# Kernel optimization log

Hardware: AMD Instinct MI355X
Metric: run time of the kernel (lower is better)

The kernel has to match this reference:

```python
import jax, jax.numpy as jnp
import numpy as np

N, E, F_IN, HID, HEADS, G = 50000, 800000, 128, 128, 4, 512
NEG_SLOPE = 0.2


def setup_inputs() -> dict:
    key = jax.random.key(0)
    ks = jax.random.split(key, 16)
    x = jax.random.normal(ks[0], (N, F_IN), dtype=jnp.float32)
    edge_index = jax.random.randint(ks[1], (2, E), 0, N, dtype=jnp.int32)
    batch = jnp.sort(jax.random.randint(ks[2], (N,), 0, G, dtype=jnp.int32))
    s1 = 1.0 / np.sqrt(F_IN)
    s2 = 1.0 / np.sqrt(HEADS * HID)
    params = {
        "W1": jax.random.uniform(ks[3], (F_IN, HEADS * HID), jnp.float32, -s1, s1),
        "a_src1": jax.random.normal(ks[4], (HEADS, HID), jnp.float32) * s1,
        "a_dst1": jax.random.normal(ks[5], (HEADS, HID), jnp.float32) * s1,
        "b1": jnp.zeros((HEADS * HID,), jnp.float32),
        "W2": jax.random.uniform(ks[6], (HEADS * HID, HID), jnp.float32, -s2, s2),
        "a_src2": jax.random.normal(ks[7], (1, HID), jnp.float32) * s2,
        "a_dst2": jax.random.normal(ks[8], (1, HID), jnp.float32) * s2,
        "b2": jnp.zeros((HID,), jnp.float32),
        "Wl": jax.random.normal(ks[9], (HID, 1), jnp.float32) / np.sqrt(HID),
        "bl": jnp.zeros((1,), jnp.float32),
    }
    return dict(x=x, edge_index=edge_index, batch=batch, **params)


def _gat_conv(x, W, a_src, a_dst, b, src, dst, heads, out_ch):
    n = x.shape[0]
    h = (x @ W).reshape(n, heads, out_ch)                      # [N,H,C]
    asrc = jnp.sum(h * a_src, axis=-1)                          # [N,H]
    adst = jnp.sum(h * a_dst, axis=-1)                          # [N,H]
    logits = jax.nn.leaky_relu(asrc[src] + adst[dst], NEG_SLOPE)  # [E,H]
    m = jax.ops.segment_max(logits, dst, num_segments=n)        # stable softmax per dst
    e = jnp.exp(logits - m[dst])
    denom = jax.ops.segment_sum(e, dst, num_segments=n)
    alpha = e / denom[dst]                                      # [E,H]
    out = jax.ops.segment_sum(alpha[:, :, None] * h[src], dst, num_segments=n)
    return out.reshape(n, heads * out_ch) + b


def reference(x, edge_index, batch, W1, a_src1, a_dst1, b1, W2, a_src2, a_dst2, b2, Wl, bl):
    n = x.shape[0]
    loop = jnp.arange(n, dtype=edge_index.dtype)
    src = jnp.concatenate([edge_index[0], loop])  # add_self_loops=True (PyG default)
    dst = jnp.concatenate([edge_index[1], loop])
    h = _gat_conv(x, W1, a_src1, a_dst1, b1, src, dst, HEADS, HID)
    h = jax.nn.elu(h)
    h = _gat_conv(h, W2, a_src2, a_dst2, b2, src, dst, 1, HID)
    h = jax.nn.elu(h)
    # global_mean_pool
    sums = jax.ops.segment_sum(h, batch, num_segments=G)
    cnts = jax.ops.segment_sum(jnp.ones((n,), h.dtype), batch, num_segments=G)
    pooled = sums / jnp.maximum(cnts, 1.0)[:, None]
    return (pooled @ Wl + bl).squeeze()
```

## Files before the change

### kernel.cpp

```cpp
#include <hip/hip_runtime.h>
#include <math.h>

#define NEG_SLOPE 0.2f

typedef float f4 __attribute__((ext_vector_type(4)));
typedef __attribute__((ext_vector_type(8))) short short8;
typedef __attribute__((ext_vector_type(4))) float f32x4;
typedef unsigned short ushort_t;
typedef unsigned char uchar_t;

__device__ __forceinline__ float bf2f(unsigned short s) {
    unsigned u = ((unsigned)s) << 16;
    float f; __builtin_memcpy(&f, &u, 4); return f;
}
__device__ __forceinline__ unsigned short f2bf(float f) {
    unsigned u; __builtin_memcpy(&u, &f, 4);
    u = (u + 0x7FFFu + ((u >> 16) & 1u)) >> 16;
    return (unsigned short)u;
}
__device__ __forceinline__ void gload16(const void* g, void* l) {
    __builtin_amdgcn_global_load_lds((const __attribute__((address_space(1))) void*)g,
                                     (__attribute__((address_space(3))) void*)l, 16, 0, 0);
}
__device__ __forceinline__ void cvt4(unsigned u, float& a, float& b, float& c, float& d) {
    asm("v_cvt_f32_ubyte0 %0, %1" : "=v"(a) : "v"(u));
    asm("v_cvt_f32_ubyte1 %0, %1" : "=v"(b) : "v"(u));
    asm("v_cvt_f32_ubyte2 %0, %1" : "=v"(c) : "v"(u));
    asm("v_cvt_f32_ubyte3 %0, %1" : "=v"(d) : "v"(u));
}

__global__ void prep_kernel(const float* __restrict__ x, const float* __restrict__ W1,
                            const float* __restrict__ W2, ushort_t* __restrict__ xb,
                            ushort_t* __restrict__ W1t, ushort_t* __restrict__ W2t,
                            const int* __restrict__ ei, int* __restrict__ deg,
                            int n_x, int pad_x, int E, int Et) {
    int i = blockIdx.x * blockDim.x + threadIdx.x;
    if (i < Et) {
        int d = (i < E) ? ei[E + i] : (i - E);
        atomicAdd(&deg[d], 1);
    }
    if (i < pad_x) {
        xb[i] = f2bf(i < n_x ? x[i] : 0.f);
        return;
    }
    int k = i - pad_x;
    if (k < 128 * 512) {
        int r = k >> 9, c = k & 511;
        W1t[(size_t)c * 128 + r] = f2bf(W1[k]);
        return;
    }
    k -= 128 * 512;
    if (k < 512 * 128) {
        int r = k >> 7, c = k & 127;
        W2t[(size_t)c * 512 + r] = f2bf(W2[k]);
    }
}

__global__ __launch_bounds__(1024) void scan_local(const int* __restrict__ deg,
                                                   int* __restrict__ off,
                                                   int* __restrict__ btot, int n) {
    __shared__ int s_w[16];
    int tid = threadIdx.x, lane = tid & 63, wv = tid >> 6;
    int i = blockIdx.x * 1024 + tid;
    int v = (i < n) ? deg[i] : 0;
    int x = v;
    #pragma unroll
    for (int d = 1; d < 64; d <<= 1) {
        int y = __shfl_up(x, d);
        if (lane >= d) x += y;
    }
    if (lane == 63) s_w[wv] = x;
    __syncthreads();
    if (tid < 16) {
        int y = s_w[tid];
        int z = y;
        #pragma unroll
        for (int d = 1; d < 16; d <<= 1) {
            int t2 = __shfl_up(z, d);
            if (tid >= d) z += t2;
        }
        if (tid == 15) btot[blockIdx.x] = z;
        s_w[tid] = z - y;
    }
    __syncthreads();
    if (i < n) off[i] = s_w[wv] + (x - v);
}

__global__ __launch_bounds__(256) void scan_add(const int* __restrict__ btot,
                                                int* __restrict__ off,
                                                int* __restrict__ cur,
                                                const int* __restrict__ batch,
                                                int* __restrict__ gcnt, int n, int nb) {
    __shared__ int s_b[2];
    int i = blockIdx.x * 256 + threadIdx.x;
    if (threadIdx.x < 64) {
        int lane = threadIdx.x;
        int v = (lane < nb) ? btot[lane] : 0;
        int x = v;
        #pragma unroll
        for (int d = 1; d < 64; d <<= 1) {
            int y = __shfl_up(x, d);
            if (lane >= d) x += y;
        }
        int c = blockIdx.x >> 2;
        int base = (c == 0) ? 0 : __shfl(x, c - 1);
        int total = __shfl(x, nb - 1);
        if (lane == 0) { s_b[0] = base; s_b[1] = total; }
    }
    __syncthreads();
    if (i < n) {
        int o = off[i] + s_b[0];
        off[i] = o;
        cur[i] = o;
        atomicAdd(&gcnt[batch[i]], 1);
    } else if (i == n) {
        off[n] = s_b[1];
    }
}

__global__ void scatter_kernel(const int* __restrict__ ei, int E, int Et,
                               int* __restrict__ cur, int* __restrict__ csr) {
    int e = blockIdx.x * blockDim.x + threadIdx.x;
    if (e >= Et) return;
    int s, d;
    if (e < E) { s = ei[e]; d = ei[E + e]; }
    else       { s = d = e - E; }
    int p = atomicAdd(&cur[d], 1);
    csr[p] = s;
}

template<int MI, int H>
__global__ __launch_bounds__(256) void gemm_q(const ushort_t* __restrict__ A,
                                              const ushort_t* __restrict__ Bt,
                                              uchar_t* __restrict__ Cq,
                                              const float* __restrict__ aw_src,
                                              const float* __restrict__ aw_dst,
                                              float* __restrict__ side,
                                              float* __restrict__ avd,
                                              int K) {
    constexpr int BM = MI * 32;
    constexpr int AI = MI / 2;
    const int Nc = H * 128;
    __shared__ __align__(16) ushort_t As[BM * 32];
    __shared__ __align__(16) ushort_t Bs[128 * 32];
    __shared__ float s_red[3][2][BM];
    __shared__ float s_rs[BM];
    __shared__ __align__(16) uchar_t s_q[BM * 144];
    const int t = threadIdx.x, w = t >> 6, lane = t & 63;
    const int r0 = blockIdx.x * BM, hb = blockIdx.y, c0 = hb * 128;
    const int wr = w & 1, wc = w >> 1;

    const ushort_t* Ag = A + (size_t)(r0 + w * (BM / 4) + (lane >> 2)) * K + (lane & 3) * 8;
    const ushort_t* Bg = Bt + (size_t)(c0 + w * 32 + (lane >> 2)) * K + (lane & 3) * 8;
    ushort_t* Al = As + w * (BM / 4) * 32;
    ushort_t* Bl = Bs + w * 1024;

    f32x4 acc[MI][4] = {};
    for (int k0 = 0; k0 < K; k0 += 32) {
        __syncthreads();
        #pragma unroll
        for (int m = 0; m < AI; m++) gload16(Ag + k0 + (size_t)m * 16 * K, Al + m * 512);
        gload16(Bg + k0, Bl);
        gload16(Bg + k0 + (size_t)16 * K, Bl + 512);
        __syncthreads();
        short8 af[MI], bf[4];
        #pragma unroll
        for (int i = 0; i < MI; i++)
            af[i] = *(const short8*)(As + (wr * MI * 16 + i * 16 + (lane & 15)) * 32 + (lane >> 4) * 8);
        #pragma unroll
        for (int jj = 0; jj < 4; jj++)
            bf[jj] = *(const short8*)(Bs + (wc * 64 + jj * 16 + (lane & 15)) * 32 + (lane >> 4) * 8);
        #pragma unroll
        for (int i = 0; i < MI; i++)
            #pragma unroll
            for (int jj = 0; jj < 4; jj++)
                acc[i][jj] = __builtin_amdgcn_mfma_f32_16x16x32_bf16(af[i], bf[jj], acc[i][jj], 0, 0, 0);
    }

    float asc[4], adc[4];
    #pragma unroll
    for (int jj = 0; jj < 4; jj++) {
        int c = c0 + wc * 64 + jj * 16 + (lane & 15);
        asc[jj] = aw_src[c];
        adc[jj] = aw_dst[c];
    }
    #pragma unroll
    for (int i = 0; i < MI; i++) {
        #pragma unroll
        for (int r = 0; r < 4; r++) {
            float m = 0.f, ps = 0.f, pd = 0.f;
            #pragma unroll
            for (int jj = 0; jj < 4; jj++) {
                float v = acc[i][jj][r];
                m = fmaxf(m, fabsf(v));
                ps = fmaf(v, asc[jj], ps);
                pd = fmaf(v, adc[jj], pd);
            }
            #pragma unroll
            for (int d = 1; d < 16; d <<= 1) {
                m = fmaxf(m, __shfl_xor(m, d));
                ps += __shfl_xor(ps, d);
                pd += __shfl_xor(pd, d);
            }
            if ((lane & 15) == 0) {
                int row = wr * MI * 16 + i * 16 + (lane >> 4) * 4 + r;
                s_red[0][wc][row] = m;
                s_red[1][wc][row] = ps;
                s_red[2][wc][row] = pd;
            }
        }
    }
    __syncthreads();
    if (t < BM) {
        float rm = fmaxf(fmaxf(s_red[0][0][t], s_red[0][1][t]), 1e-30f);
        s_rs[t] = 127.f / rm;
        int node = r0 + t;
        side[(size_t)node * (2 * H) + hb]     = s_red[1][0][t] + s_red[1][1][t];
        side[(size_t)node * (2 * H) + H + hb] = rm * (1.f / 127.f);
        avd[(size_t)node * H + hb]            = s_red[2][0][t] + s_red[2][1][t];
    }
    __syncthreads();
    #pragma unroll
    for (int i = 0; i < MI; i++)
        #pragma unroll
        for (int jj = 0; jj < 4; jj++)
            #pragma unroll
            for (int r = 0; r < 4; r++) {
                int row = wr * MI * 16 + i * 16 + (lane >> 4) * 4 + r;
                int col = wc * 64 + jj * 16 + (lane & 15);
                int qi = (int)rintf(acc[i][jj][r] * s_rs[row]) + 128;
                qi = min(255, max(0, qi));
                s_q[row * 144 + col] = (uchar_t)qi;
            }
    __syncthreads();
    #pragma unroll
    for (int p2 = 0; p2 < BM / 32; p2++) {
        int idx = p2 * 256 + t;
        int row = idx >> 3, ch = idx & 7;
        *(uint4*)(Cq + (size_t)(r0 + row) * Nc + c0 + ch * 16) =
            *(const uint4*)(s_q + row * 144 + ch * 16);
    }
}

template<int H, int TOT>
__global__ __launch_bounds__(256) void agg_q(const int* __restrict__ off,
                                             const int* __restrict__ csr,
                                             const uchar_t* __restrict__ fq,
                                             const float* __restrict__ side,
                                             const float* __restrict__ avd,
                                             const float* __restrict__ bias,
                                             ushort_t* __restrict__ outb,
                                             float* __restrict__ outf, int n) {
    constexpr int J = TOT / 64;
    __shared__ __align__(16) float2 s_w[4][64 * H];
    int w = threadIdx.x >> 6, lane = threadIdx.x & 63;
    int dst = blockIdx.x * 4 + w;
    if (dst >= n) return;
    float adv[H];
    if constexpr (H == 4) {
        f4 t4 = *(const f4*)&avd[(size_t)dst * 4];
        #pragma unroll
        for (int h = 0; h < 4; h++) adv[h] = t4[h];
    } else {
        adv[0] = avd[dst];
    }
    int beg = off[dst], end = off[dst + 1];
    float den = 0.f, Ssum = 0.f;
    float acc[16] = {};
    float2* eww = s_w[w];

    const int half = lane >> 5, sub32 = lane & 31;
    const int hch  = sub32 >> 3;
    const int slot = lane >> 3, sub8 = lane & 7;

    for (int b = beg; b < end; b += 64) {
        int idx = b + lane;
        bool val = idx < end;
        int sv = val ? csr[idx] : 0;
        unsigned myoff = (unsigned)sv * TOT;
        int cnt = min(64, end - b);

        if constexpr (J == 8) {
            uint4 A[4], B[4];
            auto issue = [&](int p0, uint4* buf) {
                #pragma unroll
                for (int q = 0; q < 4; q++) {
                    unsigned o = (unsigned)__shfl((int)myoff, (p0 + q) * 2 + half);
                    buf[q] = *(const uint4*)(fq + o + sub32 * 16);
                }
            };
            int np = (cnt + 1) >> 1;
            int ng = (np + 3) >> 2;
            issue(0, A);
            {
                const f4* sp = (const f4*)(side + (size_t)sv * 8);
                f4 av = sp[0], sc = sp[1];
                f4 ev, esv;
                #pragma unroll
                for (int h = 0; h < 4; h++) {
                    float l = av[h] + adv[h];
                    l = fmaxf(l, l * NEG_SLOPE);
                    float e = val ? __expf(l) : 0.f;
                    ev[h] = e;
                    esv[h] = e * sc[h];
                }
                f4 v01 = {ev[0], esv[0], ev[1], esv[1]};
                f4 v23 = {ev[2], esv[2], ev[3], esv[3]};
                *(f4*)&eww[lane * 4]     = v01;
                *(f4*)&eww[lane * 4 + 2] = v23;
            }
            asm volatile("s_waitcnt lgkmcnt(0)" ::: "memory");
            auto proc = [&](int p0, uint4* buf) {
                #pragma unroll
                for (int q = 0; q < 4; q++) {
                    float2 ees = eww[((p0 + q) * 2 + half) * 4 + hch];
                    den += ees.x; Ssum += ees.y;
                    float es = ees.y;
                    float b0, b1, b2, b3;
                    cvt4(buf[q].x, b0, b1, b2, b3);
                    acc[0] = fmaf(es, b0, acc[0]);  acc[1] = fmaf(es, b1, acc[1]);
                    acc[2] = fmaf(es, b2, acc[2]);  acc[3] = fmaf(es, b3, acc[3]);
                    cvt4(buf[q].y, b0, b1, b2, b3);
                    acc[4] = fmaf(es, b0, acc[4]);  acc[5] = fmaf(es, b1, acc[5]);
                    acc[6] = fmaf(es, b2, acc[6]);  acc[7] = fmaf(es, b3, acc[7]);
                    cvt4(buf[q].z, b0, b1, b2, b3);
                    acc[8] = fmaf(es, b0, acc[8]);  acc[9] = fmaf(es, b1, acc[9]);
                    acc[10] = fmaf(es, b2, acc[10]); acc[11] = fmaf(es, b3, acc[11]);
                    cvt4(buf[q].w, b0, b1, b2, b3);
                    acc[12] = fmaf(es, b0, acc[12]); acc[13] = fmaf(es, b1, acc[13]);
                    acc[14] = fmaf(es, b2, acc[14]); acc[15] = fmaf(es, b3, acc[15]);
                }
            };
            int g = 0;
            for (;;) {
                if (g + 1 < ng) issue((g + 1) * 4, B);
                proc(g * 4, A);
                if (++g >= ng) break;
                if (g + 1 < ng) issue((g + 1) * 4, A);
                proc(g * 4, B);
                if (++g >= ng) break;
            }
        } else {
            {
                float2 sp = *(const float2*)(side + (size_t)sv * 2);
                float l = sp.x + adv[0];
                l = fmaxf(l, l * NEG_SLOPE);
                float e = val ? __expf(l) : 0.f;
                eww[lane] = make_float2(e, e * sp.y);
            }
            asm volatile("s_waitcnt lgkmcnt(0)" ::: "memory");
            int ng = (cnt + 7) >> 3;
            uint4 bufs[8];
            #pragma unroll
            for (int g = 0; g < 8; g++) {
                if (g < ng) {
                    unsigned o = (unsigned)__shfl((int)myoff, g * 8 + slot);
                    bufs[g] = *(const uint4*)(fq + o + sub8 * 16);
                }
            }
            #pragma unroll
            for (int g = 0; g < 8; g++) {
                if (g < ng) {
                    float2 ees = eww[g * 8 + slot];
                    den += ees.x; Ssum += ees.y;
                    float es = ees.y;
                    float b0, b1, b2, b3;
                    cvt4(bufs[g].x, b0, b1, b2, b3);
                    acc[0] = fmaf(es, b0, acc[0]);  acc[1] = fmaf(es, b1, acc[1]);
                    acc[2] = fmaf(es, b2, acc[2]);  acc[3] = fmaf(es, b3, acc[3]);
                    cvt4(bufs[g].y, b0, b1, b2, b3);
                    acc[4] = fmaf(es, b0, acc[4]);  acc[5] = fmaf(es, b1, acc[5]);
                    acc[6] = fmaf(es, b2, acc[6]);  acc[7] = fmaf(es, b3, acc[7]);
                    cvt4(bufs[g].z, b0, b1, b2, b3);
                    acc[8] = fmaf(es, b0, acc[8]);  acc[9] = fmaf(es, b1, acc[9]);
                    acc[10] = fmaf(es, b2, acc[10]); acc[11] = fmaf(es, b3, acc[11]);
                    cvt4(bufs[g].w, b0, b1, b2, b3);
                    acc[12] = fmaf(es, b0, acc[12]); acc[13] = fmaf(es, b1, acc[13]);
                    acc[14] = fmaf(es, b2, acc[14]); acc[15] = fmaf(es, b3, acc[15]);
                }
            }
        }
    }

    if constexpr (J == 8) {
        den += __shfl_xor(den, 32);
        Ssum += __shfl_xor(Ssum, 32);
        #pragma unroll
        for (int u = 0; u < 16; u++) acc[u] += __shfl_xor(acc[u], 32);
        float rden = 1.f / den;
        if (half == 0) {
            unsigned short ov[16];
            #pragma unroll
            for (int u = 0; u < 16; u++) {
                float v = (acc[u] - 128.f * Ssum) * rden + bias[sub32 * 16 + u];
                v = v > 0.f ? v : expm1f(v);
                ov[u] = f2bf(v);
            }
            ushort_t* op = outb + (size_t)dst * TOT + sub32 * 16;
            *(short8*)op = *(short8*)ov;
            *(short8*)(op + 8) = *(short8*)(ov + 8);
        }
    } else {
        #pragma unroll
        for (int d = 8; d < 64; d <<= 1) {
            den += __shfl_xor(den, d);
            Ssum += __shfl_xor(Ssum, d);
        }
        #pragma unroll
        for (int u = 0; u < 16; u++) {
            #pragma unroll
            for (int d = 8; d < 64; d <<= 1) acc[u] += __shfl_xor(acc[u], d);
        }
        float rden = 1.f / den;
        if (lane < 8) {
            float ov[16];
            #pragma unroll
            for (int u = 0; u < 16; u++) {
                float v = (acc[u] - 128.f * Ssum) * rden + bias[lane * 16 + u];
                ov[u] = v > 0.f ? v : expm1f(v);
            }
            float* op = outf + (size_t)dst * TOT + lane * 16;
            #pragma unroll
            for (int q = 0; q < 4; q++)
                *(f4*)(op + q * 4) = *(f4*)(ov + q * 4);
        }
    }
}

__global__ __launch_bounds__(256) void pool_kernel(const float* __restrict__ feat,
                                                   const int* __restrict__ batch,
                                                   float* __restrict__ gsum, int n) {
    int t = threadIdx.x;
    int ch = t & 127, half = t >> 7;
    int base = blockIdx.x * 64;
    float acc = 0.f;
    int curg = -1;
    for (int k = half; k < 64; k += 2) {
        int node = base + k;
        if (node >= n) break;
        int g = batch[node];
        if (g != curg) {
            if (curg >= 0) atomicAdd(&gsum[(size_t)curg * 128 + ch], acc);
            acc = 0.f;
            curg = g;
        }
        acc += feat[(size_t)node * 128 + ch];
    }
    if (curg >= 0) atomicAdd(&gsum[(size_t)curg * 128 + ch], acc);
}

__global__ __launch_bounds__(256) void final_kernel(const float* __restrict__ gsum,
                                                    const int* __restrict__ gcnt,
                                                    const float* __restrict__ Wl,
                                                    const float* __restrict__ bl,
                                                    float* __restrict__ out, int g_total) {
    int w = threadIdx.x >> 6, lane = threadIdx.x & 63;
    int g = blockIdx.x * 4 + w;
    if (g >= g_total) return;
    float inv = 1.f / fmaxf((float)gcnt[g], 1.f);
    float p = 0.f;
    #pragma unroll
    for (int j = 0; j < 2; j++) {
        int ch = lane + 64 * j;
        p += gsum[(size_t)g * 128 + ch] * Wl[ch];
    }
    #pragma unroll
    for (int d = 32; d; d >>= 1) p += __shfl_xor(p, d);
    if (lane == 0) out[g] = p * inv + bl[0];
}

extern "C" void kernel_launch(void* const* d_in, const int* in_sizes, int n_in,
                              void* d_out, int out_size, void* d_ws, size_t ws_size,
                              hipStream_t stream) {
    const float* x   = (const float*)d_in[0];
    const int*   ei  = (const int*)d_in[1];
    const int*   bat = (const int*)d_in[2];
    const float* W1  = (const float*)d_in[3];
    const float* as1 = (const float*)d_in[4];
    const float* ad1 = (const float*)d_in[5];
    const float* b1  = (const float*)d_in[6];
    const float* W2  = (const float*)d_in[7];
    const float* as2 = (const float*)d_in[8];
    const float* ad2 = (const float*)d_in[9];
    const float* b2  = (const float*)d_in[10];
    const float* Wl  = (const float*)d_in[11];
    const float* bl  = (const float*)d_in[12];
    float* out = (float*)d_out;

    const int N    = in_sizes[0] / 128;
    const int E    = in_sizes[1] / 2;
    const int Et   = E + N;
    const int G    = 512;
    const int Mpad = (N + 127) & ~127;
    const int nb   = (N + 1023) >> 10;

    char* p = (char*)d_ws;
    auto alloc = [&](size_t bytes) { char* r = p; p += (bytes + 255) & ~(size_t)255; return r; };
    ushort_t* xb    = (ushort_t*)alloc((size_t)Mpad * 128 * 2);
    ushort_t* W1t   = (ushort_t*)alloc((size_t)512 * 128 * 2);
    ushort_t* W2t   = (ushort_t*)alloc((size_t)128 * 512 * 2);
    uchar_t*  h1q   = (uchar_t*)alloc((size_t)Mpad * 512);
    ushort_t* hb    = (ushort_t*)alloc((size_t)Mpad * 512 * 2);
    uchar_t*  h2q   = (uchar_t*)alloc((size_t)Mpad * 128);
    float*    feat2 = (float*)alloc((size_t)N * 128 * 4);
    float*    side1 = (float*)alloc((size_t)Mpad * 8 * 4);
    float*    avd1  = (float*)alloc((size_t)Mpad * 4 * 4);
    float*    side2 = (float*)alloc((size_t)Mpad * 2 * 4);
    float*    avd2  = (float*)alloc((size_t)Mpad * 4);
    float*    gsum  = (float*)alloc((size_t)G * 128 * 4);
    int*      gcnt  = (int*)alloc((size_t)G * 4);
    int*      deg   = (int*)alloc((size_t)N * 4);
    int*      off   = (int*)alloc((size_t)(N + 1) * 4);
    int*      cur   = (int*)alloc((size_t)N * 4);
    int*      btot  = (int*)alloc((size_t)128 * 4);
    int*      csr   = (int*)alloc((size_t)Et * 4);

    hipMemsetAsync(gsum, 0, (size_t)((char*)off - (char*)gsum), stream);
    hipMemsetAsync(hb + (size_t)N * 512, 0, (size_t)(Mpad - N) * 512 * 2, stream);

    const int prep_n = Mpad * 128 + 2 * 65536;
    prep_kernel<<<(prep_n + 255) / 256, 256, 0, stream>>>(x, W1, W2, xb, W1t, W2t,
                                                          ei, deg, N * 128, Mpad * 128, E, Et);
    scan_local<<<nb, 1024, 0, stream>>>(deg, off, btot, N);
    scan_add<<<(N + 256) / 256, 256, 0, stream>>>(btot, off, cur, bat, gcnt, N, nb);
    scatter_kernel<<<(Et + 255) / 256, 256, 0, stream>>>(ei, E, Et, cur, csr);

    gemm_q<4, 4><<<dim3(Mpad / 128, 4), 256, 0, stream>>>(xb, W1t, h1q, as1, ad1, side1, avd1, 128);
    agg_q<4, 512><<<(N + 3) / 4, 256, 0, stream>>>(off, csr, h1q, side1, avd1, b1, hb, nullptr, N);

    gemm_q<2, 1><<<dim3(Mpad / 64, 1), 256, 0, stream>>>(hb, W2t, h2q, as2, ad2, side2, avd2, 512);
    agg_q<1, 128><<<(N + 3) / 4, 256, 0, stream>>>(off, csr, h2q, side2, avd2, b2, nullptr, feat2, N);

    pool_kernel<<<(N + 63) / 64, 256, 0, stream>>>(feat2, bat, gsum, N);
    final_kernel<<<(G + 3) / 4, 256, 0, stream>>>(gsum, gcnt, Wl, bl, out, G);
}
```

Baseline: 513.3 us.

## Store layer-1 quantized features head-major and split aggregation per head

The layer-1 GEMM now writes int8 features in a head-major layout ([H][Mpad][128]) and interleaves side data per head. Layer-1 aggregation is split across a grid y-dimension of 4 heads, each warp gathering 128-byte rows for one head instead of 512-byte rows for all heads. This shrinks the gathered working set per launch so it fits cache better and adds parallelism. In exchange, the CSR indices and side data are reread four times and the double-buffered prefetch pipeline is replaced by simpler batched loads.

```diff
diff --git a/kernel.cpp b/kernel.cpp
--- a/kernel.cpp
+++ b/kernel.cpp
@@ -9,10 +9,6 @@
 typedef unsigned short ushort_t;
 typedef unsigned char uchar_t;
 
-__device__ __forceinline__ float bf2f(unsigned short s) {
-    unsigned u = ((unsigned)s) << 16;
-    float f; __builtin_memcpy(&f, &u, 4); return f;
-}
 __device__ __forceinline__ unsigned short f2bf(float f) {
     unsigned u; __builtin_memcpy(&u, &f, 4);
     u = (u + 0x7FFFu + ((u >> 16) & 1u)) >> 16;
@@ -137,10 +133,9 @@
                                               const float* __restrict__ aw_dst,
                                               float* __restrict__ side,
                                               float* __restrict__ avd,
-                                              int K) {
+                                              int K, int Mpad) {
     constexpr int BM = MI * 32;
     constexpr int AI = MI / 2;
-    const int Nc = H * 128;
     __shared__ __align__(16) ushort_t As[BM * 32];
     __shared__ __align__(16) ushort_t Bs[128 * 32];
     __shared__ float s_red[3][2][BM];
@@ -215,8 +210,8 @@
         float rm = fmaxf(fmaxf(s_red[0][0][t], s_red[0][1][t]), 1e-30f);
         s_rs[t] = 127.f / rm;
         int node = r0 + t;
-        side[(size_t)node * (2 * H) + hb]     = s_red[1][0][t] + s_red[1][1][t];
-        side[(size_t)node * (2 * H) + H + hb] = rm * (1.f / 127.f);
+        side[((size_t)node * H + hb) * 2]     = s_red[1][0][t] + s_red[1][1][t];
+        side[((size_t)node * H + hb) * 2 + 1] = rm * (1.f / 127.f);
         avd[(size_t)node * H + hb]            = s_red[2][0][t] + s_red[2][1][t];
     }
     __syncthreads();
@@ -237,142 +232,72 @@
     for (int p2 = 0; p2 < BM / 32; p2++) {
         int idx = p2 * 256 + t;
         int row = idx >> 3, ch = idx & 7;
-        *(uint4*)(Cq + (size_t)(r0 + row) * Nc + c0 + ch * 16) =
+        *(uint4*)(Cq + ((size_t)hb * Mpad + r0 + row) * 128 + ch * 16) =
             *(const uint4*)(s_q + row * 144 + ch * 16);
     }
 }
 
-template<int H, int TOT>
-__global__ __launch_bounds__(256) void agg_q(const int* __restrict__ off,
-                                             const int* __restrict__ csr,
-                                             const uchar_t* __restrict__ fq,
-                                             const float* __restrict__ side,
-                                             const float* __restrict__ avd,
-                                             const float* __restrict__ bias,
-                                             ushort_t* __restrict__ outb,
-                                             float* __restrict__ outf, int n) {
-    constexpr int J = TOT / 64;
-    __shared__ __align__(16) float2 s_w[4][64 * H];
+__global__ __launch_bounds__(256) void agg_q1(const int* __restrict__ off,
+                                              const int* __restrict__ csr,
+                                              const uchar_t* __restrict__ fq,
+                                              const float* __restrict__ side,
+                                              const float* __restrict__ avd,
+                                              const float* __restrict__ bias,
+                                              ushort_t* __restrict__ outb,
+                                              int n, int Mpad) {
+    __shared__ float2 s_w[4][64];
     int w = threadIdx.x >> 6, lane = threadIdx.x & 63;
     int dst = blockIdx.x * 4 + w;
+    int h = blockIdx.y;
     if (dst >= n) return;
-    float adv[H];
-    if constexpr (H == 4) {
-        f4 t4 = *(const f4*)&avd[(size_t)dst * 4];
-        #pragma unroll
-        for (int h = 0; h < 4; h++) adv[h] = t4[h];
-    } else {
-        adv[0] = avd[dst];
-    }
+    float adv = avd[(size_t)dst * 4 + h];
     int beg = off[dst], end = off[dst + 1];
     float den = 0.f, Ssum = 0.f;
     float acc[16] = {};
     float2* eww = s_w[w];
-
-    const int half = lane >> 5, sub32 = lane & 31;
-    const int hch  = sub32 >> 3;
     const int slot = lane >> 3, sub8 = lane & 7;
+    const uchar_t* fqh = fq + (size_t)h * Mpad * 128;
 
     for (int b = beg; b < end; b += 64) {
         int idx = b + lane;
         bool val = idx < end;
         int sv = val ? csr[idx] : 0;
-        unsigned myoff = (unsigned)sv * TOT;
+        unsigned myoff = (unsigned)sv * 128;
+        {
+            float2 sp = *(const float2*)(side + ((size_t)sv * 4 + h) * 2);
+            float l = sp.x + adv;
+            l = fmaxf(l, l * NEG_SLOPE);
+            float e = val ? __expf(l) : 0.f;
+            eww[lane] = make_float2(e, e * sp.y);
+        }
+        asm volatile("s_waitcnt lgkmcnt(0)" ::: "memory");
         int cnt = min(64, end - b);
-
-        if constexpr (J == 8) {
-            uint4 A[4], B[4];
-            auto issue = [&](int p0, uint4* buf) {
-                #pragma unroll
-                for (int q = 0; q < 4; q++) {
-                    unsigned o = (unsigned)__shfl((int)myoff, (p0 + q) * 2 + half);
-                    buf[q] = *(const uint4*)(fq + o + sub32 * 16);
+        int ng = (cnt + 7) >> 3;
+        for (int g0 = 0; g0 < ng; g0 += 4) {
+            uint4 bufs[4];
+            int gm = min(4, ng - g0);
+            #pragma unroll
+            for (int g = 0; g < 4; g++) {
+                if (g < gm) {
+                    unsigned o = (unsigned)__shfl((int)myoff, (g0 + g) * 8 + slot);
+                    bufs[g] = *(const uint4*)(fqh + o + sub8 * 16);
                 }
-            };
-            int np = (cnt + 1) >> 1;
-            int ng = (np + 3) >> 2;
-            issue(0, A);
-            {
-                const f4* sp = (const f4*)(side + (size_t)sv * 8);
-                f4 av = sp[0], sc = sp[1];
-                f4 ev, esv;
-                #pragma unroll
-                for (int h = 0; h < 4; h++) {
-                    float l = av[h] + adv[h];
-                    l = fmaxf(l, l * NEG_SLOPE);
-                    float e = val ? __expf(l) : 0.f;
-                    ev[h] = e;
-                    esv[h] = e * sc[h];
-                }
-                f4 v01 = {ev[0], esv[0], ev[1], esv[1]};
-                f4 v23 = {ev[2], esv[2], ev[3], esv[3]};
-                *(f4*)&eww[lane * 4]     = v01;
-                *(f4*)&eww[lane * 4 + 2] = v23;
-            }
-            asm volatile("s_waitcnt lgkmcnt(0)" ::: "memory");
-            auto proc = [&](int p0, uint4* buf) {
-                #pragma unroll
-                for (int q = 0; q < 4; q++) {
-                    float2 ees = eww[((p0 + q) * 2 + half) * 4 + hch];
-                    den += ees.x; Ssum += ees.y;
-                    float es = ees.y;
-                    float b0, b1, b2, b3;
-                    cvt4(buf[q].x, b0, b1, b2, b3);
-                    acc[0] = fmaf(es, b0, acc[0]);  acc[1] = fmaf(es, b1, acc[1]);
-                    acc[2] = fmaf(es, b2, acc[2]);  acc[3] = fmaf(es, b3, acc[3]);
-                    cvt4(buf[q].y, b0, b1, b2, b3);
-                    acc[4] = fmaf(es, b0, acc[4]);  acc[5] = fmaf(es, b1, acc[5]);
-                    acc[6] = fmaf(es, b2, acc[6]);  acc[7] = fmaf(es, b3, acc[7]);
-                    cvt4(buf[q].z, b0, b1, b2, b3);
-                    acc[8] = fmaf(es, b0, acc[8]);  acc[9] = fmaf(es, b1, acc[9]);
-                    acc[10] = fmaf(es, b2, acc[10]); acc[11] = fmaf(es, b3, acc[11]);
-                    cvt4(buf[q].w, b0, b1, b2, b3);
-                    acc[12] = fmaf(es, b0, acc[12]); acc[13] = fmaf(es, b1, acc[13]);
-                    acc[14] = fmaf(es, b2, acc[14]); acc[15] = fmaf(es, b3, acc[15]);
-                }
-            };
-            int g = 0;
-            for (;;) {
-                if (g + 1 < ng) issue((g + 1) * 4, B);
-                proc(g * 4, A);
-                if (++g >= ng) break;
-                if (g + 1 < ng) issue((g + 1) * 4, A);
-                proc(g * 4, B);
-                if (++g >= ng) break;
-            }
-        } else {
-            {
-                float2 sp = *(const float2*)(side + (size_t)sv * 2);
-                float l = sp.x + adv[0];
-                l = fmaxf(l, l * NEG_SLOPE);
-                float e = val ? __expf(l) : 0.f;
-                eww[lane] = make_float2(e, e * sp.y);
-            }
-            asm volatile("s_waitcnt lgkmcnt(0)" ::: "memory");
-            int ng = (cnt + 7) >> 3;
-            uint4 bufs[8];
-            #pragma unroll
-            for (int g = 0; g < 8; g++) {
-                if (g < ng) {
-                    unsigned o = (unsigned)__shfl((int)myoff, g * 8 + slot);
-                    bufs[g] = *(const uint4*)(fq + o + sub8 * 16);
-                }
-            }
-            #pragma unroll
-            for (int g = 0; g < 8; g++) {
-                if (g < ng) {
-                    float2 ees = eww[g * 8 + slot];
+            }
+            #pragma unroll
+            for (int g = 0; g < 4; g++) {
+                if (g < gm) {
+                    float2 ees = eww[(g0 + g) * 8 + slot];
                     den += ees.x; Ssum += ees.y;
                     float es = ees.y;
                     float b0, b1, b2, b3;
                     cvt4(bufs[g].x, b0, b1, b2, b3);
-                    acc[0] = fmaf(es, b0, acc[0]);  acc[1] = fmaf(es, b1, acc[1]);
-                    acc[2] = fmaf(es, b2, acc[2]);  acc[3] = fmaf(es, b3, acc[3]);
+                    acc[0] = fmaf(es, b0, acc[0]);   acc[1] = fmaf(es, b1, acc[1]);
+                    acc[2] = fmaf(es, b2, acc[2]);   acc[3] = fmaf(es, b3, acc[3]);
                     cvt4(bufs[g].y, b0, b1, b2, b3);
-                    acc[4] = fmaf(es, b0, acc[4]);  acc[5] = fmaf(es, b1, acc[5]);
-                    acc[6] = fmaf(es, b2, acc[6]);  acc[7] = fmaf(es, b3, acc[7]);
+                    acc[4] = fmaf(es, b0, acc[4]);   acc[5] = fmaf(es, b1, acc[5]);
+                    acc[6] = fmaf(es, b2, acc[6]);   acc[7] = fmaf(es, b3, acc[7]);
                     cvt4(bufs[g].z, b0, b1, b2, b3);
-                    acc[8] = fmaf(es, b0, acc[8]);  acc[9] = fmaf(es, b1, acc[9]);
+                    acc[8] = fmaf(es, b0, acc[8]);   acc[9] = fmaf(es, b1, acc[9]);
                     acc[10] = fmaf(es, b2, acc[10]); acc[11] = fmaf(es, b3, acc[11]);
                     cvt4(bufs[g].w, b0, b1, b2, b3);
                     acc[12] = fmaf(es, b0, acc[12]); acc[13] = fmaf(es, b1, acc[13]);
@@ -381,49 +306,119 @@
             }
         }
     }
-
-    if constexpr (J == 8) {
-        den += __shfl_xor(den, 32);
-        Ssum += __shfl_xor(Ssum, 32);
-        #pragma unroll
-        for (int u = 0; u < 16; u++) acc[u] += __shfl_xor(acc[u], 32);
-        float rden = 1.f / den;
-        if (half == 0) {
-            unsigned short ov[16];
-            #pragma unroll
-            for (int u = 0; u < 16; u++) {
-                float v = (acc[u] - 128.f * Ssum) * rden + bias[sub32 * 16 + u];
-                v = v > 0.f ? v : expm1f(v);
-                ov[u] = f2bf(v);
-            }
-            ushort_t* op = outb + (size_t)dst * TOT + sub32 * 16;
-            *(short8*)op = *(short8*)ov;
-            *(short8*)(op + 8) = *(short8*)(ov + 8);
-        }
-    } else {
-        #pragma unroll
-        for (int d = 8; d < 64; d <<= 1) {
-            den += __shfl_xor(den, d);
-            Ssum += __shfl_xor(Ssum, d);
-        }
+    #pragma unroll
+    for (int d = 8; d < 64; d <<= 1) {
+        den += __shfl_xor(den, d);
+        Ssum += __shfl_xor(Ssum, d);
+    }
+    #pragma unroll
+    for (int u = 0; u < 16; u++) {
+        #pragma unroll
+        for (int d = 8; d < 64; d <<= 1) acc[u] += __shfl_xor(acc[u], d);
+    }
+    float rden = 1.f / den;
+    if (lane < 8) {
+        unsigned short ov[16];
         #pragma unroll
         for (int u = 0; u < 16; u++) {
-            #pragma unroll
-            for (int d = 8; d < 64; d <<= 1) acc[u] += __shfl_xor(acc[u], d);
-        }
-        float rden = 1.f / den;
-        if (lane < 8) {
-            float ov[16];
-            #pragma unroll
-            for (int u = 0; u < 16; u++) {
-                float v = (acc[u] - 128.f * Ssum) * rden + bias[lane * 16 + u];
-                ov[u] = v > 0.f ? v : expm1f(v);
-            }
-            float* op = outf + (size_t)dst * TOT + lane * 16;
-            #pragma unroll
-            for (int q = 0; q < 4; q++)
-                *(f4*)(op + q * 4) = *(f4*)(ov + q * 4);
-        }
+            float v = (acc[u] - 128.f * Ssum) * rden + bias[h * 128 + lane * 16 + u];
+            v = v > 0.f ? v : expm1f(v);
+            ov[u] = f2bf(v);
+        }
+        ushort_t* op = outb + (size_t)dst * 512 + h * 128 + lane * 16;
+        *(short8*)op = *(short8*)ov;
+        *(short8*)(op + 8) = *(short8*)(ov + 8);
+    }
+}
+
+__global__ __launch_bounds__(256) void agg_q2(const int* __restrict__ off,
+                                              const int* __restrict__ csr,
+                                              const uchar_t* __restrict__ fq,
+                                              const float* __restrict__ side,
+                                              const float* __restrict__ avd,
+                                              const float* __restrict__ bias,
+                                              float* __restrict__ outf, int n) {
+    __shared__ float2 s_w[4][64];
+    int w = threadIdx.x >> 6, lane = threadIdx.x & 63;
+    int dst = blockIdx.x * 4 + w;
+    if (dst >= n) return;
+    float adv = avd[dst];
+    int beg = off[dst], end = off[dst + 1];
+    float den = 0.f, Ssum = 0.f;
+    float acc[16] = {};
+    float2* eww = s_w[w];
+    const int slot = lane >> 3, sub8 = lane & 7;
+
+    for (int b = beg; b < end; b += 64) {
+        int idx = b + lane;
+        bool val = idx < end;
+        int sv = val ? csr[idx] : 0;
+        unsigned myoff = (unsigned)sv * 128;
+        {
+            float2 sp = *(const float2*)(side + (size_t)sv * 2);
+            float l = sp.x + adv;
+            l = fmaxf(l, l * NEG_SLOPE);
+            float e = val ? __expf(l) : 0.f;
+            eww[lane] = make_float2(e, e * sp.y);
+        }
+        asm volatile("s_waitcnt lgkmcnt(0)" ::: "memory");
+        int cnt = min(64, end - b);
+        int ng = (cnt + 7) >> 3;
+        for (int g0 = 0; g0 < ng; g0 += 4) {
+            uint4 bufs[4];
+            int gm = min(4, ng - g0);
+            #pragma unroll
+            for (int g = 0; g < 4; g++) {
+                if (g < gm) {
+                    unsigned o = (unsigned)__shfl((int)myoff, (g0 + g) * 8 + slot);
+                    bufs[g] = *(const uint4*)(fq + o + sub8 * 16);
+                }
+            }
+            #pragma unroll
+            for (int g = 0; g < 4; g++) {
+                if (g < gm) {
+                    float2 ees = eww[(g0 + g) * 8 + slot];
+                    den += ees.x; Ssum += ees.y;
+                    float es = ees.y;
+                    float b0, b1, b2, b3;
+                    cvt4(bufs[g].x, b0, b1, b2, b3);
+                    acc[0] = fmaf(es, b0, acc[0]);   acc[1] = fmaf(es, b1, acc[1]);
+                    acc[2] = fmaf(es, b2, acc[2]);   acc[3] = fmaf(es, b3, acc[3]);
+                    cvt4(bufs[g].y, b0, b1, b2, b3);
+                    acc[4] = fmaf(es, b0, acc[4]);   acc[5] = fmaf(es, b1, acc[5]);
+                    acc[6] = fmaf(es, b2, acc[6]);   acc[7] = fmaf(es, b3, acc[7]);
+                    cvt4(bufs[g].z, b0, b1, b2, b3);
+                    acc[8] = fmaf(es, b0, acc[8]);   acc[9] = fmaf(es, b1, acc[9]);
+                    acc[10] = fmaf(es, b2, acc[10]); acc[11] = fmaf(es, b3, acc[11]);
+                    cvt4(bufs[g].w, b0, b1, b2, b3);
+                    acc[12] = fmaf(es, b0, acc[12]); acc[13] = fmaf(es, b1, acc[13]);
+                    acc[14] = fmaf(es, b2, acc[14]); acc[15] = fmaf(es, b3, acc[15]);
+                }
+            }
+        }
+    }
+    #pragma unroll
+    for (int d = 8; d < 64; d <<= 1) {
+        den += __shfl_xor(den, d);
+        Ssum += __shfl_xor(Ssum, d);
+    }
+    #pragma unroll
+    for (int u = 0; u < 16; u++) {
+        #pragma unroll
+        for (int d = 8; d < 64; d <<= 1) acc[u] += __shfl_xor(acc[u], d);
+    }
+    float rden = 1.f / den;
+    if (lane < 8) {
+        float ov[16];
+        #pragma unroll
+        for (int u = 0; u < 16; u++) {
+            float v = (acc[u] - 128.f * Ssum) * rden + bias[lane * 16 + u];
+            ov[u] = v > 0.f ? v : expm1f(v);
+        }
+        float* op = outf + (size_t)dst * 128 + lane * 16;
+        #pragma unroll
+        for (int q = 0; q < 4; q++)
+            *(f4*)(op + q * 4) = *(f4*)(ov + q * 4);
     }
 }
 
@@ -525,11 +520,13 @@
     scan_add<<<(N + 256) / 256, 256, 0, stream>>>(btot, off, cur, bat, gcnt, N, nb);
     scatter_kernel<<<(Et + 255) / 256, 256, 0, stream>>>(ei, E, Et, cur, csr);
 
-    gemm_q<4, 4><<<dim3(Mpad / 128, 4), 256, 0, stream>>>(xb, W1t, h1q, as1, ad1, side1, avd1, 128);
-    agg_q<4, 512><<<(N + 3) / 4, 256, 0, stream>>>(off, csr, h1q, side1, avd1, b1, hb, nullptr, N);
-
-    gemm_q<2, 1><<<dim3(Mpad / 64, 1), 256, 0, stream>>>(hb, W2t, h2q, as2, ad2, side2, avd2, 512);
-    agg_q<1, 128><<<(N + 3) / 4, 256, 0, stream>>>(off, csr, h2q, side2, avd2, b2, nullptr, feat2, N);
+    gemm_q<4, 4><<<dim3(Mpad / 128, 4), 256, 0, stream>>>(xb, W1t, h1q, as1, ad1, side1, avd1,
+                                                          128, Mpad);
+    agg_q1<<<dim3((N + 3) / 4, 4), 256, 0, stream>>>(off, csr, h1q, side1, avd1, b1, hb, N, Mpad);
+
+    gemm_q<2, 1><<<dim3(Mpad / 64, 1), 256, 0, stream>>>(hb, W2t, h2q, as2, ad2, side2, avd2,
+                                                         512, Mpad);
+    agg_q2<<<(N + 3) / 4, 256, 0, stream>>>(off, csr, h2q, side2, avd2, b2, feat2, N);
 
     pool_kernel<<<(N + 63) / 64, 256, 0, stream>>>(feat2, bat, gsum, N);
     final_kernel<<<(G + 3) / 4, 256, 0, stream>>>(gsum, gcnt, Wl, bl, out, G);
```

Result: slower. 624.1 us (+21.6%).
